# Kernel tuning notes

Hardware: AMD Instinct MI355X
Metric: run time of the kernel (lower is better)

## Reference

```python
import jax, jax.numpy as jnp
import numpy as np

RETRIEVAL_NUM = 80
THRESHOLD = 0.5


def setup_inputs() -> dict:
    key = jax.random.key(0)
    ks = jax.random.split(key, 6)
    B, N, D = 256, 100, 768
    return {
        "mean_pooling_vec": jax.random.normal(ks[0], (B, D), dtype=jnp.float32),
        "merge_text_vec": jax.random.normal(ks[1], (B, D), dtype=jnp.float32),
        "retrieved_visual_feature_embedding_cls": jax.random.normal(ks[2], (B, N, 1, D), dtype=jnp.float32),
        "retrieved_textual_feature_embedding": jax.random.normal(ks[3], (B, N, 1, D), dtype=jnp.float32),
        "retrieved_label_list": jax.random.normal(ks[4], (B, N), dtype=jnp.float32),
        "RRCP": jax.random.uniform(ks[5], (B, N), dtype=jnp.float32),
    }


def _ragged_pack(feats, binary, counts):
    # feats: [B, R, D]; binary: [B, R] int; counts: [B]
    # Stable sort so that valid (binary==1) positions come first in original order,
    # matching torch.where(RRCP[i]==1)[0] followed by front-packing.
    order = jnp.argsort(1 - binary, axis=1)  # default stable sort: valid idx first
    packed = jnp.take_along_axis(feats, order[:, :, None], axis=1)
    keep = (jnp.arange(feats.shape[1])[None, :] < counts[:, None])  # [B, R]
    return packed * keep[:, :, None].astype(feats.dtype)


def reference(mean_pooling_vec, merge_text_vec, retrieved_visual_feature_embedding_cls,
              retrieved_textual_feature_embedding, retrieved_label_list, RRCP):
    R = RETRIEVAL_NUM
    vis = jnp.squeeze(retrieved_visual_feature_embedding_cls, 2)[:, :R, :]  # [B,R,D]
    txt = jnp.squeeze(retrieved_textual_feature_embedding, 2)[:, :R, :]    # [B,R,D]
    rr = RRCP[:, :R]
    labels = retrieved_label_list[:, :R]

    binary = (rr > THRESHOLD).astype(jnp.int32)  # [B,R]
    rr_mod = jnp.where(rr < THRESHOLD, 0.0, rr)
    zero_rows = jnp.all(rr_mod == 0.0, axis=1)
    rr_mod = rr_mod.at[:, 0].set(jnp.where(zero_rows, 1.0, rr_mod[:, 0]))

    counts = binary.sum(axis=1)  # valid nodes per row, [B]
    vis_packed = _ragged_pack(vis, binary, counts)
    txt_packed = _ragged_pack(txt, binary, counts)

    B = rr.shape[0]
    pos = jnp.arange(R + 1)
    text_mask = (pos[None, :] <= counts[:, None]).astype(jnp.float32)  # [B,R+1]
    # Faithful to the source bug: img_mask is only zeroed for the LAST batch row
    # (the loop-variable `i` leaks out of the python loop in preprocess_data).
    img_mask = jnp.ones((B, R + 1), dtype=jnp.float32)
    img_mask = img_mask.at[B - 1].set((pos <= counts[B - 1]).astype(jnp.float32))

    # graph_attention is external/undefined in the given source; the kernel-headroom
    # target is the ragged gather/pad pipeline, whose outputs we return.
    return (vis_packed, txt_packed, text_mask, img_mask, rr_mod, labels)
```

## Files before the change

### kernel.cpp

```cpp
#include <hip/hip_runtime.h>
#include <hip/hip_bf16.h>

#define B   256
#define N   100
#define D   768
#define R   80
#define THRESHOLD 0.5f

#define SZ_VIS   ((long)B * R * D)
#define OFF_VIS  0L
#define OFF_TXT  (OFF_VIS + SZ_VIS)
#define OFF_TMASK (OFF_TXT + SZ_VIS)
#define OFF_IMASK (OFF_TMASK + (long)B*(R+1))
#define OFF_RR    (OFF_IMASK + (long)B*(R+1))
#define OFF_LAB   (OFF_RR + (long)B*R)

__global__ __launch_bounds__(128) void prep_kernel(
    const float* __restrict__ rr_in,
    const float* __restrict__ lab_in,
    float* __restrict__ out,
    int* __restrict__ order,
    int* __restrict__ counts)
{
    const int b = blockIdx.x;
    const int t = threadIdx.x;

    __shared__ float rrs[R];
    __shared__ int   bin[R];
    __shared__ int   cnt_s;
    __shared__ int   zero_s;

    if (t < R) {
        float v = rr_in[b * N + t];
        rrs[t] = v;
        bin[t] = (v > THRESHOLD) ? 1 : 0;
        out[OFF_LAB + (long)b * R + t] = lab_in[b * N + t];
    }
    __syncthreads();

    if (t == 0) {
        int c = 0;
        for (int i = 0; i < R; ++i)
            if (bin[i]) order[b * R + c++] = i;
        int p = c;
        for (int i = 0; i < R; ++i)
            if (!bin[i]) order[b * R + p++] = i;
        cnt_s = c;
        counts[b] = c;
        int allz = 1;
        for (int i = 0; i < R; ++i) {
            float rm = (rrs[i] < THRESHOLD) ? 0.0f : rrs[i];
            if (rm != 0.0f) { allz = 0; break; }
        }
        zero_s = allz;
    }
    __syncthreads();

    const int cnt = cnt_s;
    if (t < R) {
        float v = rrs[t];
        float rm = (v < THRESHOLD) ? 0.0f : v;
        if (t == 0 && zero_s) rm = 1.0f;
        out[OFF_RR + (long)b * R + t] = rm;
    }
    if (t <= R) {
        float tm = (t <= cnt) ? 1.0f : 0.0f;
        out[OFF_TMASK + (long)b * (R + 1) + t] = tm;
        float im = (b == B - 1) ? tm : 1.0f;
        out[OFF_IMASK + (long)b * (R + 1) + t] = im;
    }
}

__global__ __launch_bounds__(192) void gather_kernel(
    const float* __restrict__ vis,
    const float* __restrict__ txt,
    float* __restrict__ out,
    const int* __restrict__ order,
    const int* __restrict__ counts)
{
    const int row = blockIdx.x;
    const int b = row / R;
    const int r = row - b * R;
    const int t = threadIdx.x;

    float4 v = make_float4(0.f, 0.f, 0.f, 0.f);
    float4 x = v;
    if (r < counts[b]) {
        const int src = order[b * R + r];
        const long in_idx = ((long)b * N + src) * D + t * 4;
        v = *(const float4*)(vis + in_idx);
        x = *(const float4*)(txt + in_idx);
    }
    const long o = ((long)b * R + r) * D + t * 4;
    *(float4*)(out + OFF_VIS + o) = v;
    *(float4*)(out + OFF_TXT + o) = x;
}

extern "C" void kernel_launch(void* const* d_in, const int* in_sizes, int n_in,
                              void* d_out, int out_size, void* d_ws, size_t ws_size,
                              hipStream_t stream) {
    const float* vis = (const float*)d_in[2];
    const float* txt = (const float*)d_in[3];
    const float* lab = (const float*)d_in[4];
    const float* rr  = (const float*)d_in[5];
    float* out = (float*)d_out;

    int* order  = (int*)d_ws;
    int* counts = order + B * R;

    prep_kernel<<<B, 128, 0, stream>>>(rr, lab, out, order, counts);
    gather_kernel<<<B * R, 192, 0, stream>>>(vis, txt, out, order, counts);
}
```

Before: 243.4 us.

## Fuse prep and gather into one kernel with per-block redundant compaction

Merges the prep and gather kernels into a single launch. Each block redundantly recomputes the row's threshold compaction in shared memory for its 8 output rows, which removes the workspace order/count round trip and the dependency between two kernels. Each block now copies 8 rows instead of 1, giving fewer, larger blocks. The cost is a serial 80-iteration scan by one thread in every block before any loads are issued.

```diff
diff --git a/kernel.cpp b/kernel.cpp
--- a/kernel.cpp
+++ b/kernel.cpp
@@ -5,95 +5,84 @@
 #define N   100
 #define D   768
 #define R   80
+#define RPB 8
 #define THRESHOLD 0.5f
 
-#define SZ_VIS   ((long)B * R * D)
-#define OFF_VIS  0L
-#define OFF_TXT  (OFF_VIS + SZ_VIS)
+#define SZ_VIS    ((long)B * R * D)
+#define OFF_VIS   0L
+#define OFF_TXT   (OFF_VIS + SZ_VIS)
 #define OFF_TMASK (OFF_TXT + SZ_VIS)
 #define OFF_IMASK (OFF_TMASK + (long)B*(R+1))
 #define OFF_RR    (OFF_IMASK + (long)B*(R+1))
 #define OFF_LAB   (OFF_RR + (long)B*R)
 
-__global__ __launch_bounds__(128) void prep_kernel(
+__global__ __launch_bounds__(192) void fused_kernel(
+    const float* __restrict__ vis,
+    const float* __restrict__ txt,
+    const float* __restrict__ lab_in,
     const float* __restrict__ rr_in,
-    const float* __restrict__ lab_in,
-    float* __restrict__ out,
-    int* __restrict__ order,
-    int* __restrict__ counts)
+    float* __restrict__ out)
 {
-    const int b = blockIdx.x;
-    const int t = threadIdx.x;
+    const int b  = blockIdx.y;
+    const int r0 = blockIdx.x * RPB;
+    const int t  = threadIdx.x;
 
     __shared__ float rrs[R];
-    __shared__ int   bin[R];
+    __shared__ int   order_s[RPB];
     __shared__ int   cnt_s;
     __shared__ int   zero_s;
 
-    if (t < R) {
-        float v = rr_in[b * N + t];
-        rrs[t] = v;
-        bin[t] = (v > THRESHOLD) ? 1 : 0;
-        out[OFF_LAB + (long)b * R + t] = lab_in[b * N + t];
-    }
+    if (t < R) rrs[t] = rr_in[b * N + t];
     __syncthreads();
 
     if (t == 0) {
         int c = 0;
-        for (int i = 0; i < R; ++i)
-            if (bin[i]) order[b * R + c++] = i;
-        int p = c;
-        for (int i = 0; i < R; ++i)
-            if (!bin[i]) order[b * R + p++] = i;
-        cnt_s = c;
-        counts[b] = c;
         int allz = 1;
         for (int i = 0; i < R; ++i) {
-            float rm = (rrs[i] < THRESHOLD) ? 0.0f : rrs[i];
-            if (rm != 0.0f) { allz = 0; break; }
+            float v = rrs[i];
+            if (v >= THRESHOLD) allz = 0;
+            if (v > THRESHOLD) {
+                int rel = c - r0;
+                if (rel >= 0 && rel < RPB) order_s[rel] = i;
+                c++;
+            }
         }
+        cnt_s  = c;
         zero_s = allz;
     }
     __syncthreads();
 
     const int cnt = cnt_s;
-    if (t < R) {
-        float v = rrs[t];
-        float rm = (v < THRESHOLD) ? 0.0f : v;
-        if (t == 0 && zero_s) rm = 1.0f;
-        out[OFF_RR + (long)b * R + t] = rm;
+
+    #pragma unroll
+    for (int j = 0; j < RPB; ++j) {
+        const int r = r0 + j;
+        float4 v = make_float4(0.f, 0.f, 0.f, 0.f);
+        float4 x = v;
+        if (r < cnt) {
+            const long in_idx = ((long)b * N + order_s[j]) * D + t * 4;
+            v = *(const float4*)(vis + in_idx);
+            x = *(const float4*)(txt + in_idx);
+        }
+        const long o = ((long)b * R + r) * D + t * 4;
+        *(float4*)(out + OFF_VIS + o) = v;
+        *(float4*)(out + OFF_TXT + o) = x;
     }
-    if (t <= R) {
-        float tm = (t <= cnt) ? 1.0f : 0.0f;
-        out[OFF_TMASK + (long)b * (R + 1) + t] = tm;
-        float im = (b == B - 1) ? tm : 1.0f;
-        out[OFF_IMASK + (long)b * (R + 1) + t] = im;
+
+    if (r0 == 0) {
+        if (t < R) {
+            out[OFF_LAB + (long)b * R + t] = lab_in[b * N + t];
+            float v  = rrs[t];
+            float rm = (v < THRESHOLD) ? 0.0f : v;
+            if (t == 0 && zero_s) rm = 1.0f;
+            out[OFF_RR + (long)b * R + t] = rm;
+        }
+        if (t <= R) {
+            float tm = (t <= cnt) ? 1.0f : 0.0f;
+            out[OFF_TMASK + (long)b * (R + 1) + t] = tm;
+            out[OFF_IMASK + (long)b * (R + 1) + t] = (b == B - 1) ? tm : 1.0f;
+        }
     }
-}
-
-__global__ __launch_bounds__(192) void gather_kernel(
-    const float* __restrict__ vis,
-    const float* __restrict__ txt,
-    float* __restrict__ out,
-    const int* __restrict__ order,
-    const int* __restrict__ counts)
-{
-    const int row = blockIdx.x;
-    const int b = row / R;
-    const int r = row - b * R;
-    const int t = threadIdx.x;
-
-    float4 v = make_float4(0.f, 0.f, 0.f, 0.f);
-    float4 x = v;
-    if (r < counts[b]) {
-        const int src = order[b * R + r];
-        const long in_idx = ((long)b * N + src) * D + t * 4;
-        v = *(const float4*)(vis + in_idx);
-        x = *(const float4*)(txt + in_idx);
-    }
-    const long o = ((long)b * R + r) * D + t * 4;
-    *(float4*)(out + OFF_VIS + o) = v;
-    *(float4*)(out + OFF_TXT + o) = x;
 }
 
 extern "C" void kernel_launch(void* const* d_in, const int* in_sizes, int n_in,
@@ -105,9 +94,6 @@
     const float* rr  = (const float*)d_in[5];
     float* out = (float*)d_out;
 
-    int* order  = (int*)d_ws;
-    int* counts = order + B * R;
-
-    prep_kernel<<<B, 128, 0, stream>>>(rr, lab, out, order, counts);
-    gather_kernel<<<B * R, 192, 0, stream>>>(vis, txt, out, order, counts);
+    dim3 grid(R / RPB, B);
+    fused_kernel<<<grid, 192, 0, stream>>>(vis, txt, lab, rr, out);
 }
```

After: 241.0 us. No clear change (-1.0%).
